# Kernel tuning notes

Measured on AMD Instinct MI355X. Metric: run time of the kernel, lower is better.

## Reference

```python
import jax, jax.numpy as jnp
import numpy as np
from jax import lax

B = 8          # batch
IMG = 224      # image size
PATCH = 16     # patch size / stride
D = 384        # embed_dim = d_model = d_inner (expand=1)
DEPTH = 24     # number of blocks
N = 16         # d_state
K = 4          # d_conv
R = 24         # dt_rank = ceil(D/16)
H = D * 4 * 2 // 3   # SwiGLU hidden = 1024
L = (IMG // PATCH) ** 2  # 196 tokens


def setup_inputs() -> dict:
    ks = iter(jax.random.split(jax.random.key(0), 40))
    def rn(shape, s=0.02):
        return jax.random.normal(next(ks), shape, jnp.float32) * s
    inp = {}
    inp["x"] = jax.random.normal(next(ks), (B, 3, IMG, IMG), jnp.float32)
    inp["patch_w"] = rn((D, 3, PATCH, PATCH))
    inp["patch_b"] = jnp.zeros((D,), jnp.float32)
    inp["norm1_w"] = jnp.ones((DEPTH, D), jnp.float32)
    inp["norm1_b"] = jnp.zeros((DEPTH, D), jnp.float32)
    inp["in_proj_w"] = rn((DEPTH, 2 * D, D))
    inp["conv_w"] = rn((DEPTH, D, K), 0.1)
    inp["conv_b"] = jnp.zeros((DEPTH, D), jnp.float32)
    inp["x_proj_w"] = rn((DEPTH, R + 2 * N, D))
    inp["dt_proj_w"] = rn((DEPTH, D, R), 0.1)
    inp["dt_proj_b"] = rn((DEPTH, D), 0.1)
    # S4D-real init: A = -exp(A_log), A_log = log(1..N)
    inp["A_log"] = jnp.tile(jnp.log(jnp.arange(1, N + 1, dtype=jnp.float32))[None, None, :], (DEPTH, D, 1))
    inp["D_skip"] = jnp.ones((DEPTH, D), jnp.float32)
    inp["out_proj_w"] = rn((DEPTH, D, D))
    inp["norm2_w"] = jnp.ones((DEPTH, D), jnp.float32)
    inp["norm2_b"] = jnp.zeros((DEPTH, D), jnp.float32)
    inp["w1_w"] = rn((DEPTH, H, D)); inp["w1_b"] = jnp.zeros((DEPTH, H), jnp.float32)
    inp["w2_w"] = rn((DEPTH, H, D)); inp["w2_b"] = jnp.zeros((DEPTH, H), jnp.float32)
    inp["w3_w"] = rn((DEPTH, D, H)); inp["w3_b"] = jnp.zeros((DEPTH, D), jnp.float32)
    inp["normf_w"] = jnp.ones((D,), jnp.float32)
    inp["normf_b"] = jnp.zeros((D,), jnp.float32)
    return inp


def _ln(x, w, b, eps=1e-5):
    m = x.mean(-1, keepdims=True)
    v = jnp.mean((x - m) ** 2, axis=-1, keepdims=True)
    return (x - m) / jnp.sqrt(v + eps) * w + b


def _mamba(x, in_w, cw, cb, xp_w, dtw, dtb, a_log, d_skip, ow):
    # x: [B, L, D]; Mamba with expand=1, bimamba 'none'
    bsz, seq, _ = x.shape
    xz = jnp.einsum('bld,ed->ble', x, in_w)        # [B, L, 2D]
    xc, z = jnp.split(xz, 2, axis=-1)
    # causal depthwise conv1d, kernel K, padding K-1, truncated to L
    xpd = jnp.pad(xc, ((0, 0), (K - 1, 0), (0, 0)))
    xconv = sum(xpd[:, k:k + seq, :] * cw[:, k] for k in range(K)) + cb
    xa = jax.nn.silu(xconv)
    dbc = jnp.einsum('bld,ed->ble', xa, xp_w)      # [B, L, R+2N]
    dt = jax.nn.softplus(jnp.einsum('blr,dr->bld', dbc[..., :R], dtw) + dtb)  # [B, L, D]
    Bm = dbc[..., R:R + N]                         # [B, L, N]
    Cm = dbc[..., R + N:]                          # [B, L, N]
    A = -jnp.exp(a_log)                            # [D, N]

    def step(h, t):
        dt_t, B_t, C_t, x_t = t                    # [B,D],[B,N],[B,N],[B,D]
        h = h * jnp.exp(dt_t[..., None] * A) + (dt_t * x_t)[..., None] * B_t[:, None, :]
        return h, jnp.einsum('bdn,bn->bd', h, C_t)

    h0 = jnp.zeros((bsz, D, N), x.dtype)
    _, ys = lax.scan(step, h0, (dt.transpose(1, 0, 2), Bm.transpose(1, 0, 2),
                                Cm.transpose(1, 0, 2), xa.transpose(1, 0, 2)))
    y = ys.transpose(1, 0, 2) + d_skip * xa
    y = y * jax.nn.silu(z)
    return jnp.einsum('bld,ed->ble', y, ow)


def _forward(x, patch_w, patch_b, norm1_w, norm1_b, in_proj_w, conv_w, conv_b,
             x_proj_w, dt_proj_w, dt_proj_b, A_log, D_skip, out_proj_w,
             norm2_w, norm2_b, w1_w, w1_b, w2_w, w2_b, w3_w, w3_b, normf_w, normf_b):
    p = lax.conv_general_dilated(x, patch_w, (PATCH, PATCH), 'VALID',
                                 dimension_numbers=('NCHW', 'OIHW', 'NCHW'))
    p = p + patch_b[None, :, None, None]
    h = p.reshape(p.shape[0], D, -1).transpose(0, 2, 1)   # [B, L, D]
    for i in range(DEPTH):
        h = h + _mamba(_ln(h, norm1_w[i], norm1_b[i]), in_proj_w[i], conv_w[i], conv_b[i],
                       x_proj_w[i], dt_proj_w[i], dt_proj_b[i], A_log[i], D_skip[i], out_proj_w[i])
        hn = _ln(h, norm2_w[i], norm2_b[i])
        hid = jax.nn.silu(hn @ w1_w[i].T + w1_b[i]) * (hn @ w2_w[i].T + w2_b[i])
        h = h + hid @ w3_w[i].T + w3_b[i]
    return _ln(h, normf_w, normf_b)


def reference(x, patch_w, patch_b, norm1_w, norm1_b, in_proj_w, conv_w, conv_b,
              x_proj_w, dt_proj_w, dt_proj_b, A_log, D_skip, out_proj_w,
              norm2_w, norm2_b, w1_w, w1_b, w2_w, w2_b, w3_w, w3_b, normf_w, normf_b):
    return _forward(x, patch_w, patch_b, norm1_w, norm1_b, in_proj_w, conv_w, conv_b,
                    x_proj_w, dt_proj_w, dt_proj_b, A_log, D_skip, out_proj_w,
                    norm2_w, norm2_b, w1_w, w1_b, w2_w, w2_b, w3_w, w3_b, normf_w, normf_b)
```

## Files before the change

kernel.cpp:

```cpp
#include <hip/hip_runtime.h>
#include <math.h>

#define BB 8
#define LL 196
#define DD 384
#define NDEPTH 24
#define NST 16
#define RRANK 24
#define HHID 1024
#define MROWS (BB*LL)
#define NCH 28
#define CHL 7

typedef float f32x4 __attribute__((ext_vector_type(4)));
typedef short s16x8 __attribute__((ext_vector_type(8)));
typedef short s16x4 __attribute__((ext_vector_type(4)));
typedef __bf16 b16x8 __attribute__((ext_vector_type(8)));
typedef unsigned short u16;
typedef unsigned int u32;

#if defined(__has_builtin)
#  if __has_builtin(__builtin_amdgcn_global_load_lds)
#    define HAS_GLL 1
#  endif
#endif
#ifndef HAS_GLL
#  define HAS_GLL 0
#endif

__device__ __forceinline__ float sigmoidf_(float x){ return 1.f/(1.f+__expf(-x)); }

__device__ __forceinline__ u16 f2bf(float f){
    u32 u = __builtin_bit_cast(u32, f);
    u32 r = (u + 0x7fffu + ((u >> 16) & 1u)) >> 16;
    return (u16)r;
}
__device__ __forceinline__ float bf2f(u16 v){
    u32 u = ((u32)v) << 16;
    return __builtin_bit_cast(float, u);
}

__device__ __forceinline__ void gll16(const u16* g, void* lds){
#if HAS_GLL
    __builtin_amdgcn_global_load_lds(
        (const __attribute__((address_space(1))) unsigned int*)g,
        (__attribute__((address_space(3))) unsigned int*)lds, 16, 0, 0);
#endif
}

template<typename V>
__device__ __forceinline__ auto mfma_try(V a, V b, f32x4 c, int)
    -> decltype(__builtin_amdgcn_mfma_f32_16x16x32_bf16(a, b, c, 0, 0, 0))
{ return __builtin_amdgcn_mfma_f32_16x16x32_bf16(a, b, c, 0, 0, 0); }

template<typename V>
__device__ __forceinline__ f32x4 mfma_try(V a, V b, f32x4 c, long)
{
    return __builtin_amdgcn_mfma_f32_16x16x32_bf16(
        __builtin_bit_cast(b16x8, a), __builtin_bit_cast(b16x8, b), c, 0, 0, 0);
}
__device__ __forceinline__ f32x4 mfma_bf16(s16x8 a, s16x8 b, f32x4 c){ return mfma_try(a, b, c, 0); }

__global__ __launch_bounds__(64) void ln_k(const float* __restrict__ X,
    const float* __restrict__ w, const float* __restrict__ b, float* __restrict__ Y)
{
    int row = blockIdx.x;
    int lane = threadIdx.x;
    const float* x = X + (size_t)row*DD;
    float v[6]; float s=0.f, s2=0.f;
    #pragma unroll
    for (int j=0;j<6;j++){ float t = x[lane + j*64]; v[j]=t; s+=t; s2+=t*t; }
    #pragma unroll
    for (int o=32;o>=1;o>>=1){ s += __shfl_xor(s,o); s2 += __shfl_xor(s2,o); }
    float m = s*(1.f/DD);
    float var = s2*(1.f/DD) - m*m;
    float rstd = rsqrtf(var + 1e-5f);
    #pragma unroll
    for (int j=0;j<6;j++){
        int c = lane + j*64;
        Y[(size_t)row*DD + c] = (v[j]-m)*rstd*w[c] + b[c];
    }
}

__global__ void gather_k(const float* __restrict__ x, u16* __restrict__ P)
{
    int idx = blockIdx.x*blockDim.x + threadIdx.x;
    if (idx >= MROWS*768) return;
    int k = idx % 768;
    int bl = idx / 768;
    int l = bl % LL;
    int b = bl / LL;
    int c = k >> 8;
    int rem = k & 255;
    int dy = rem >> 4, dx = rem & 15;
    int py = l / 14, px = l % 14;
    P[idx] = f2bf(x[(((size_t)b*3 + c)*224 + (py*16+dy))*224 + (px*16+dx)]);
}

__device__ __forceinline__ int swz(int row, int chunk){
    return (row << 7) + ((chunk ^ (row & 7)) << 4);
}

template<int EPI, bool WB, int CFG, int PRO, int K>
__global__ __launch_bounds__(256) void mgemm_k(
    const u16* __restrict__ A, const float* __restrict__ Af,
    const float* __restrict__ lnw, const float* __restrict__ lnb,
    const void* __restrict__ W1v, const void* __restrict__ W2v,
    const float* __restrict__ bias1, const float* __restrict__ bias2,
    float* __restrict__ Cf, u16* __restrict__ Cb,
    int M, int N)
{
    constexpr int  BM   = (CFG==1)?32:16;
    constexpr int  FM   = (CFG==2)?1:2;
    constexpr int  FN   = 2;
    constexpr int  NAR  = (BM+31)/32;
    constexpr bool DUAL = (EPI==4);
    constexpr int  ABY  = BM*128;
    constexpr int  BBY  = 128*128;
    constexpr bool ASY  = WB && (HAS_GLL==1);
    constexpr int  NKT  = K >> 6;
    __shared__ __attribute__((aligned(16))) char sm[2*ABY + 2*BBY + (DUAL ? 2*BBY : 0)];
    char* A0 = sm;          char* A1 = sm + ABY;
    char* B0 = sm + 2*ABY;  char* B1 = B0 + BBY;
    char* C0 = B1 + BBY;    char* C1 = C0 + BBY;

    const int tid = threadIdx.x;
    const int row0 = blockIdx.y * BM;
    const int col0 = blockIdx.x << 7;
    const int w = tid >> 6, lane = tid & 63;
    const int wn  = w;
    const int lr = lane & 15, lk = lane >> 4;
    const int ar0 = tid >> 3, ac8 = tid & 7;
    const bool apart = (CFG != 2) || (tid < 128);

    const u16*   W1b = (const u16*)W1v;
    const u16*   W2b = (const u16*)W2v;
    const float* W1f = (const float*)W1v;
    const float* W2f = (const float*)W2v;

    f32x4 acc [FM][FN] = {};
    f32x4 acc2[FM][FN] = {};

    s16x8 aval[NAR];
    s16x8 bval[4], b2val[4];
    float4 bvf[8], b2vf[8];
    s16x8 lnr[(PRO==1)?NKT:1];

    if (PRO == 1 && apart){
        const float* xrow = Af + (size_t)(row0 + ar0)*DD;
        float4 va[6], vb[6];
        float s = 0.f, s2 = 0.f;
        #pragma unroll
        for (int j=0;j<6;j++){
            va[j] = *(const float4*)(xrow + j*64 + ac8*8);
            vb[j] = *(const float4*)(xrow + j*64 + ac8*8 + 4);
            s  += va[j].x+va[j].y+va[j].z+va[j].w + vb[j].x+vb[j].y+vb[j].z+vb[j].w;
            s2 += va[j].x*va[j].x+va[j].y*va[j].y+va[j].z*va[j].z+va[j].w*va[j].w
                + vb[j].x*vb[j].x+vb[j].y*vb[j].y+vb[j].z*vb[j].z+vb[j].w*vb[j].w;
        }
        #pragma unroll
        for (int o=1;o<8;o<<=1){ s += __shfl_xor(s,o); s2 += __shfl_xor(s2,o); }
        float m = s*(1.f/DD);
        float rstd = rsqrtf(s2*(1.f/DD) - m*m + 1e-5f);
        #pragma unroll
        for (int j=0;j<6;j++){
            int c0 = j*64 + ac8*8;
            float4 w0 = *(const float4*)(lnw + c0);
            float4 w1 = *(const float4*)(lnw + c0 + 4);
            float4 b0 = *(const float4*)(lnb + c0);
            float4 b1 = *(const float4*)(lnb + c0 + 4);
            s16x8 ov;
            ov[0]=(short)f2bf((va[j].x-m)*rstd*w0.x+b0.x);
            ov[1]=(short)f2bf((va[j].y-m)*rstd*w0.y+b0.y);
            ov[2]=(short)f2bf((va[j].z-m)*rstd*w0.z+b0.z);
            ov[3]=(short)f2bf((va[j].w-m)*rstd*w0.w+b0.w);
            ov[4]=(short)f2bf((vb[j].x-m)*rstd*w1.x+b1.x);
            ov[5]=(short)f2bf((vb[j].y-m)*rstd*w1.y+b1.y);
            ov[6]=(short)f2bf((vb[j].z-m)*rstd*w1.z+b1.z);
            ov[7]=(short)f2bf((vb[j].w-m)*rstd*w1.w+b1.w);
            if (j < NKT) lnr[j] = ov;
        }
    }

    auto stageAsync = [&](int kt, char* bA, char* bB, char* bC){
        const int lhi = lane >> 3, llo = lane & 7;
        const int colel = (kt << 6) + ((llo ^ lhi) << 3);
        if (PRO == 0){
            constexpr int ACH = BM/8;
            #pragma unroll
            for (int ci = w; ci < ACH; ci += 4){
                int gr = row0 + ci*8 + lhi;
                gll16(A + (size_t)gr*K + colel, bA + ci*1024);
            }
        }
        #pragma unroll
        for (int i=0;i<4;i++){
            int ci = w*4 + i;
            int gb = col0 + ci*8 + lhi;
            gll16(W1b + (size_t)gb*K + colel, bB + ci*1024);
        }
        if (DUAL){
            #pragma unroll
            for (int i=0;i<4;i++){
                int ci = w*4 + i;
                int gb = col0 + ci*8 + lhi;
                gll16(W2b + (size_t)gb*K + colel, bC + ci*1024);
            }
        }
    };

    auto loadT = [&](int kt){
        const int kb = kt << 6;
        if (PRO == 0 && apart){
            #pragma unroll
            for (int i=0;i<NAR;i++){
                int gr = row0 + i*32 + ar0;
                if (gr < M) aval[i] = *(const s16x8*)(A + (size_t)gr*K + kb + ac8*8);
                else        aval[i] = s16x8{0,0,0,0,0,0,0,0};
            }
        }
        if (WB){
            #pragma unroll
            for (int i=0;i<4;i++){
                int gb = col0 + i*32 + ar0;
                if (gb < N) bval[i] = *(const s16x8*)(W1b + (size_t)gb*K + kb + ac8*8);
                else        bval[i] = s16x8{0,0,0,0,0,0,0,0};
            }
            if (DUAL){
                #pragma unroll
                for (int i=0;i<4;i++){
                    int gb = col0 + i*32 + ar0;
                    if (gb < N) b2val[i] = *(const s16x8*)(W2b + (size_t)gb*K + kb + ac8*8);
                    else        b2val[i] = s16x8{0,0,0,0,0,0,0,0};
                }
            }
        } else {
            #pragma unroll
            for (int i=0;i<8;i++){
                int ss = i*256 + tid;
                int r = ss >> 4, q = ss & 15;
                int gb = col0 + r;
                if (gb < N) bvf[i] = *(const float4*)(W1f + (size_t)gb*K + kb + q*4);
                else        bvf[i] = float4{0,0,0,0};
            }
            if (DUAL){
                #pragma unroll
                for (int i=0;i<8;i++){
                    int ss = i*256 + tid;
                    int r = ss >> 4, q = ss & 15;
                    int gb = col0 + r;
                    if (gb < N) b2vf[i] = *(const float4*)(W2f + (size_t)gb*K + kb + q*4);
                    else        b2vf[i] = float4{0,0,0,0};
                }
            }
        }
    };
    auto writeT = [&](char* bA, char* bB, char* bC){
        if (PRO == 0 && apart){
            #pragma unroll
            for (int i=0;i<NAR;i++)
                *(s16x8*)(bA + swz(i*32 + ar0, ac8)) = aval[i];
        }
        if (WB){
            #pragma unroll
            for (int i=0;i<4;i++)
                *(s16x8*)(bB + swz(i*32 + ar0, ac8)) = bval[i];
            if (DUAL){
                #pragma unroll
                for (int i=0;i<4;i++)
                    *(s16x8*)(bC + swz(i*32 + ar0, ac8)) = b2val[i];
            }
        } else {
            #pragma unroll
            for (int i=0;i<8;i++){
                int ss = i*256 + tid;
                int r = ss >> 4, q = ss & 15;
                float4 v = bvf[i];
                s16x4 cv = { (short)f2bf(v.x), (short)f2bf(v.y), (short)f2bf(v.z), (short)f2bf(v.w) };
                int off = (r << 7) + (((q >> 1) ^ (r & 7)) << 4) + ((q & 1) << 3);
                *(s16x4*)(bB + off) = cv;
            }
            if (DUAL){
                #pragma unroll
                for (int i=0;i<8;i++){
                    int ss = i*256 + tid;
                    int r = ss >> 4, q = ss & 15;
                    float4 v = b2vf[i];
                    s16x4 cv = { (short)f2bf(v.x), (short)f2bf(v.y), (short)f2bf(v.z), (short)f2bf(v.w) };
                    int off = (r << 7) + (((q >> 1) ^ (r & 7)) << 4) + ((q & 1) << 3);
                    *(s16x4*)(bC + off) = cv;
                }
            }
        }
    };

    auto compute = [&](char* cA, char* cB, char* cC){
        #pragma unroll
        for (int ks=0; ks<2; ks++){
            s16x8 af[FM], bfr[FN];
            #pragma unroll
            for (int m=0;m<FM;m++)
                af[m] = *(const s16x8*)(cA + swz(m*16 + lr, ks*4 + lk));
            #pragma unroll
            for (int n=0;n<FN;n++)
                bfr[n] = *(const s16x8*)(cB + swz(wn*32 + n*16 + lr, ks*4 + lk));
            #pragma unroll
            for (int m=0;m<FM;m++)
                #pragma unroll
                for (int n=0;n<FN;n++)
                    acc[m][n] = mfma_bf16(af[m], bfr[n], acc[m][n]);
            if (DUAL){
                s16x8 b2r[FN];
                #pragma unroll
                for (int n=0;n<FN;n++)
                    b2r[n] = *(const s16x8*)(cC + swz(wn*32 + n*16 + lr, ks*4 + lk));
                #pragma unroll
                for (int m=0;m<FM;m++)
                    #pragma unroll
                    for (int n=0;n<FN;n++)
                        acc2[m][n] = mfma_bf16(af[m], b2r[n], acc2[m][n]);
            }
        }
    };

    if (ASY) stageAsync(0, A0, B0, C0);
    else   { loadT(0); writeT(A0, B0, C0); }
    if (PRO == 1 && apart) *(s16x8*)(A0 + swz(ar0, ac8)) = lnr[0];
    __syncthreads();
    #pragma unroll
    for (int kt=0; kt<NKT; kt++){
        const bool more = (kt+1 < NKT);
        char* nA = (kt&1)?A0:A1; char* nB = (kt&1)?B0:B1; char* nC = (kt&1)?C0:C1;
        if (more){
            if (ASY) stageAsync(kt+1, nA, nB, nC);
            else     loadT(kt+1);
            if (PRO == 1 && apart) *(s16x8*)(nA + swz(ar0, ac8)) = lnr[(kt+1 < NKT) ? (kt+1) : 0];
        }
        if (kt & 1) compute(A1, B1, C1);
        else        compute(A0, B0, C0);
        if (more && !ASY) writeT(nA, nB, nC);
        __syncthreads();
    }

    #pragma unroll
    for (int n=0;n<FN;n++){
        int gc = col0 + wn*32 + n*16 + lr;
        if (gc >= N) continue;
        float b1 = 0.f, b2 = 0.f;
        if (EPI==1||EPI==3||EPI==4) b1 = bias1[gc];
        if (EPI==4) b2 = bias2[gc];
        #pragma unroll
        for (int m=0;m<FM;m++){
            #pragma unroll
            for (int r=0;r<4;r++){
                int gr = row0 + m*16 + lk*4 + r;
                if (gr >= M) continue;
                float v = acc[m][n][r];
                if (EPI==1||EPI==3) v += b1;
                if (EPI==2||EPI==3) v += Cf[(size_t)gr*N + gc];
                if (EPI==4){
                    float v1 = v + b1;
                    float v2 = acc2[m][n][r] + b2;
                    Cb[(size_t)gr*N + gc] = f2bf(v1 * sigmoidf_(v1) * v2);
                } else if (EPI==6){
                    Cb[(size_t)gr*N + gc] = f2bf(v);
                } else {
                    Cf[(size_t)gr*N + gc] = v;
                }
            }
        }
    }
}

template<int K>
__device__ __forceinline__ int off_a(int row, int chunk){
    return row*(K*2) + ((chunk ^ (row & 7)) << 4);
}

template<bool WB>
__global__ __launch_bounds__(256) void xproj_k(
    const u16* __restrict__ xzb,
    const float* __restrict__ cw, const float* __restrict__ cb,
    const void* __restrict__ Wv,
    float* __restrict__ dbc)
{
    constexpr int K = DD, N = 56;
    constexpr int ABY = 16*K*2;
    __shared__ __attribute__((aligned(16))) char sm[ABY + 2*16384];
    char* sA = sm;
    char* B0 = sm + ABY;
    char* B1 = B0 + 16384;

    const int tid = threadIdx.x;
    const int row0 = blockIdx.x * 16;
    const int wv = tid >> 6, lane = tid & 63;
    const int lr = lane & 15, lk = lane >> 4;
    const int ar0 = tid >> 3, ac8 = tid & 7;

    const u16*   Wb = (const u16*)Wv;
    const float* Wf = (const float*)Wv;

    f32x4 acc[2] = {};
    s16x8 bval[4];
    float4 bvf[8];

    auto loadB = [&](int kt){
        const int kb = kt << 6;
        if (WB){
            #pragma unroll
            for (int i=0;i<4;i++){
                int gb = i*32 + ar0;
                if (gb < N) bval[i] = *(const s16x8*)(Wb + (size_t)gb*K + kb + ac8*8);
                else        bval[i] = s16x8{0,0,0,0,0,0,0,0};
            }
        } else {
            #pragma unroll
            for (int i=0;i<8;i++){
                int ss = i*256 + tid;
                int r = ss >> 4, q = ss & 15;
                if (r < N) bvf[i] = *(const float4*)(Wf + (size_t)r*K + kb + q*4);
                else       bvf[i] = float4{0,0,0,0};
            }
        }
    };
    auto writeB = [&](char* bB){
        if (WB){
            #pragma unroll
            for (int i=0;i<4;i++)
                *(s16x8*)(bB + swz(i*32 + ar0, ac8)) = bval[i];
        } else {
            #pragma unroll
            for (int i=0;i<8;i++){
                int ss = i*256 + tid;
                int r = ss >> 4, q = ss & 15;
                float4 v = bvf[i];
                s16x4 cv = { (short)f2bf(v.x), (short)f2bf(v.y), (short)f2bf(v.z), (short)f2bf(v.w) };
                int off = (r << 7) + (((q >> 1) ^ (r & 7)) << 4) + ((q & 1) << 3);
                *(s16x4*)(bB + off) = cv;
            }
        }
    };

    loadB(0);

    #pragma unroll
    for (int r=0;r<4;r++){
        int rl = wv*4 + r, gr = row0 + rl;
        if (lane < 48){
            int l = gr % LL, bb = gr / LL;
            int d0 = lane*8;
            float a[8];
            #pragma unroll
            for (int j=0;j<8;j++) a[j] = cb[d0+j];
            #pragma unroll
            for (int t=0;t<4;t++){
                int ls = l - 3 + t;
                if (ls >= 0){
                    s16x8 xv = *(const s16x8*)(xzb + (size_t)(bb*LL+ls)*768 + d0);
                    #pragma unroll
                    for (int j=0;j<8;j++)
                        a[j] = fmaf(bf2f((u16)xv[j]), cw[(d0+j)*4+t], a[j]);
                }
            }
            s16x8 ov;
            #pragma unroll
            for (int j=0;j<8;j++)
                ov[j] = (short)f2bf(a[j]*sigmoidf_(a[j]));
            *(s16x8*)(sA + off_a<K>(rl, lane)) = ov;
        }
    }

    writeB(B0);
    __syncthreads();

    constexpr int nkt = K >> 6;
    #pragma unroll
    for (int kt=0; kt<nkt; kt++){
        const bool more = (kt+1 < nkt);
        if (more) loadB(kt+1);
        char* cB = (kt & 1) ? B1 : B0;
        #pragma unroll
        for (int ks=0; ks<2; ks++){
            s16x8 af = *(const s16x8*)(sA + off_a<K>(lr, kt*8 + ks*4 + lk));
            #pragma unroll
            for (int n=0;n<2;n++){
                s16x8 bfr = *(const s16x8*)(cB + swz(wv*32 + n*16 + lr, ks*4 + lk));
                acc[n] = mfma_bf16(af, bfr, acc[n]);
            }
        }
        if (more) writeB((kt & 1) ? B0 : B1);
        __syncthreads();
    }

    #pragma unroll
    for (int n=0;n<2;n++){
        int gc = wv*32 + n*16 + lr;
        if (gc >= N) continue;
        #pragma unroll
        for (int r=0;r<4;r++){
            int gr = row0 + lk*4 + r;
            dbc[(size_t)gr*N + gc] = acc[n][r];
        }
    }
}

__global__ void cvtw_k(const float* __restrict__ s, u16* __restrict__ d, int n)
{
    int i = blockIdx.x*blockDim.x + threadIdx.x;
    int idx = i*4;
    if (idx + 4 <= n){
        float4 v = *(const float4*)(s + idx);
        s16x4 cv = { (short)f2bf(v.x), (short)f2bf(v.y), (short)f2bf(v.z), (short)f2bf(v.w) };
        *(s16x4*)(d + idx) = cv;
    } else {
        for (int j=idx;j<n;j++) d[j] = f2bf(s[j]);
    }
}

__global__ __launch_bounds__(384) void scanA_k(
    const float* __restrict__ dbc, const u16* __restrict__ xzb,
    const float* __restrict__ cw, const float* __restrict__ cb,
    const float* __restrict__ dtw, const float* __restrict__ dtb,
    const float* __restrict__ a_log,
    float* __restrict__ Pout, float* __restrict__ Sout,
    float2* __restrict__ dtxv)
{
    int b = blockIdx.x / NCH;
    int c = blockIdx.x % NCH;
    int d = threadIdx.x;
    __shared__ float Ds[CHL][56];
    for (int t = threadIdx.x; t < CHL*56; t += 384){
        int j = t/56, q = t%56;
        Ds[j][q] = dbc[(size_t)(b*LL + c*CHL + j)*56 + q];
    }
    __syncthreads();
    float cwr[4];
    #pragma unroll
    for (int k=0;k<4;k++) cwr[k] = cw[d*4+k];
    float cbv = cb[d];
    float dtwr[RRANK];
    #pragma unroll
    for (int r=0;r<RRANK;r++) dtwr[r] = dtw[d*RRANK + r];
    float dtbv = dtb[d];
    float Aa[NST];
    #pragma unroll
    for (int n=0;n<NST;n++) Aa[n] = -__expf(a_log[d*NST+n]);
    int l0 = c*CHL;
    float p3=0.f, p2=0.f, p1=0.f;
    if (l0 >= 3) p3 = bf2f(xzb[(size_t)(b*LL+l0-3)*768 + d]);
    if (l0 >= 2) p2 = bf2f(xzb[(size_t)(b*LL+l0-2)*768 + d]);
    if (l0 >= 1) p1 = bf2f(xzb[(size_t)(b*LL+l0-1)*768 + d]);
    float hst[NST], P[NST];
    #pragma unroll
    for (int n=0;n<NST;n++){ hst[n]=0.f; P[n]=1.f; }
    #pragma unroll
    for (int j=0;j<CHL;j++){
        int row = b*LL + l0 + j;
        float cur = bf2f(xzb[(size_t)row*768 + d]);
        float a = cbv;
        a = fmaf(p3, cwr[0], a); a = fmaf(p2, cwr[1], a);
        a = fmaf(p1, cwr[2], a); a = fmaf(cur, cwr[3], a);
        p3 = p2; p2 = p1; p1 = cur;
        float xv = a * sigmoidf_(a);
        float t = dtbv;
        #pragma unroll
        for (int r=0;r<RRANK;r++) t = fmaf(dtwr[r], Ds[j][r], t);
        float dtv = (t > 20.f) ? t : log1pf(__expf(t));
        dtxv[(size_t)row*DD + d] = float2{dtv, xv};
        float du = dtv*xv;
        #pragma unroll
        for (int n=0;n<NST;n++){
            float e = __expf(dtv*Aa[n]);
            hst[n] = fmaf(hst[n], e, du*Ds[j][24+n]);
            P[n] *= e;
        }
    }
    size_t base = ((size_t)(b*NCH + c)*DD + d)*NST;
    #pragma unroll
    for (int n=0;n<NST;n++){ Pout[base+n]=P[n]; Sout[base+n]=hst[n]; }
}

__global__ __launch_bounds__(384) void scanC_k(
    const float* __restrict__ dbc, const float2* __restrict__ dtxv,
    const u16* __restrict__ xzb, const float* __restrict__ a_log,
    const float* __restrict__ Pin, const float* __restrict__ Sin,
    const float* __restrict__ dskip,
    u16* __restrict__ yg)
{
    int b = blockIdx.x / NCH;
    int c = blockIdx.x % NCH;
    int d = threadIdx.x;
    __shared__ float Ds[CHL][56];
    for (int t = threadIdx.x; t < CHL*56; t += 384){
        int j = t/56, q = t%56;
        Ds[j][q] = dbc[(size_t)(b*LL + c*CHL + j)*56 + q];
    }
    __syncthreads();
    float hst[NST];
    #pragma unroll
    for (int n=0;n<NST;n++) hst[n]=0.f;
    for (int cc=0; cc<c; cc++){
        size_t base = ((size_t)(b*NCH + cc)*DD + d)*NST;
        #pragma unroll
        for (int n=0;n<NST;n++)
            hst[n] = fmaf(Pin[base+n], hst[n], Sin[base+n]);
    }
    float Aa[NST];
    #pragma unroll
    for (int n=0;n<NST;n++) Aa[n] = -__expf(a_log[d*NST+n]);
    float dsk = dskip[d];
    int l0 = c*CHL;
    #pragma unroll
    for (int j=0;j<CHL;j++){
        int row = b*LL + l0 + j;
        float2 dx = dtxv[(size_t)row*DD + d];
        float dtv = dx.x, xv = dx.y;
        float du = dtv*xv;
        float y = 0.f;
        #pragma unroll
        for (int n=0;n<NST;n++){
            float e = __expf(dtv*Aa[n]);
            hst[n] = fmaf(hst[n], e, du*Ds[j][24+n]);
            y = fmaf(hst[n], Ds[j][40+n], y);
        }
        float zv = bf2f(xzb[(size_t)row*768 + 384 + d]);
        float g = zv * sigmoidf_(zv);
        yg[(size_t)row*DD + d] = f2bf((y + dsk*xv)*g);
    }
}

template<int EPI, int CFG, int PRO, int K>
static void mg(bool wb, dim3 g, hipStream_t s,
               const void* A, const float* Af, const float* lnw, const float* lnb,
               const void* Wb, const void* Wf, const void* W2b, const void* W2f,
               const float* b1, const float* b2, float* Cf, u16* Cb,
               int M, int N)
{
    if (wb) mgemm_k<EPI,true ,CFG,PRO,K><<<g,256,0,s>>>((const u16*)A, Af, lnw, lnb, Wb, W2b, b1, b2, Cf, Cb, M, N);
    else    mgemm_k<EPI,false,CFG,PRO,K><<<g,256,0,s>>>((const u16*)A, Af, lnw, lnb, Wf, W2f, b1, b2, Cf, Cb, M, N);
}

extern "C" void kernel_launch(void* const* d_in, const int* in_sizes, int n_in,
                              void* d_out, int out_size, void* d_ws, size_t ws_size,
                              hipStream_t stream)
{
    const float* x         = (const float*)d_in[0];
    const float* patch_w   = (const float*)d_in[1];
    const float* patch_b   = (const float*)d_in[2];
    const float* norm1_w   = (const float*)d_in[3];
    const float* norm1_b   = (const float*)d_in[4];
    const float* in_proj_w = (const float*)d_in[5];
    const float* conv_w    = (const float*)d_in[6];
    const float* conv_b    = (const float*)d_in[7];
    const float* x_proj_w  = (const float*)d_in[8];
    const float* dt_w      = (const float*)d_in[9];
    const float* dt_b      = (const float*)d_in[10];
    const float* A_log     = (const float*)d_in[11];
    const float* D_skip    = (const float*)d_in[12];
    const float* out_w     = (const float*)d_in[13];
    const float* norm2_w   = (const float*)d_in[14];
    const float* norm2_b   = (const float*)d_in[15];
    const float* w1_w      = (const float*)d_in[16];
    const float* w1_b      = (const float*)d_in[17];
    const float* w2_w      = (const float*)d_in[18];
    const float* w2_b      = (const float*)d_in[19];
    const float* w3_w      = (const float*)d_in[20];
    const float* w3_b      = (const float*)d_in[21];
    const float* normf_w   = (const float*)d_in[22];
    const float* normf_b   = (const float*)d_in[23];

    char* wsb = (char*)d_ws;
    size_t o = 0;
    auto take = [&](size_t bytes) -> char* {
        char* p = wsb + o;
        o += (bytes + 255) & ~(size_t)255;
        return p;
    };

    float* h    = (float*)take((size_t)602112*4);
    float* dbc  = (float*)take((size_t)87808*4);
    float* Pb   = (float*)take((size_t)BB*NCH*DD*NST*4);
    float* Sb   = (float*)take((size_t)BB*NCH*DD*NST*4);
    float2* dtxv= (float2*)take((size_t)MROWS*DD*8);
    u16*  xzb   = (u16*)take((size_t)1204224*2);
    u16*  yg    = (u16*)take((size_t)602112*2);
    u16*  hid   = (u16*)take((size_t)1605632*2);
    u16*  patches = hid;

    const size_t NPW = 294912, NIN = 7077888, NOUT = 3538944,
                 NW1 = 9437184, NW2 = 9437184, NW3 = 9437184, NXP = 516096;
    u16* wcP = (u16*)take(NPW*2);
    u16* wcI = (u16*)take(NIN*2);
    u16* wcO = (u16*)take(NOUT*2);
    u16* wc1 = (u16*)take(NW1*2);
    u16* wc2 = (u16*)take(NW2*2);
    u16* wc3 = (u16*)take(NW3*2);
    u16* wcX = (u16*)take(NXP*2);
    bool wb = (ws_size >= o);

    if (wb){
        cvtw_k<<<(int)((NPW/4+255)/256), 256, 0, stream>>>(patch_w, wcP, (int)NPW);
        cvtw_k<<<(int)((NIN/4+255)/256), 256, 0, stream>>>(in_proj_w, wcI, (int)NIN);
        cvtw_k<<<(int)((NOUT/4+255)/256),256, 0, stream>>>(out_w, wcO, (int)NOUT);
        cvtw_k<<<(int)((NW1/4+255)/256), 256, 0, stream>>>(w1_w, wc1, (int)NW1);
        cvtw_k<<<(int)((NW2/4+255)/256), 256, 0, stream>>>(w2_w, wc2, (int)NW2);
        cvtw_k<<<(int)((NW3/4+255)/256), 256, 0, stream>>>(w3_w, wc3, (int)NW3);
        cvtw_k<<<(int)((NXP/4+255)/256), 256, 0, stream>>>(x_proj_w, wcX, (int)NXP);
    }

    const int GY32 = MROWS/32;
    const int GY16 = MROWS/16;

    gather_k<<<(MROWS*768+255)/256, 256, 0, stream>>>(x, patches);
    mg<1,2,0,768>(wb, dim3(3,GY16), stream, patches, nullptr, nullptr, nullptr,
              wcP, patch_w, nullptr, nullptr, patch_b, nullptr, h, nullptr, MROWS, DD);

    for (int i=0;i<NDEPTH;i++){
        mg<6,1,1,384>(wb, dim3(6,GY32), stream, nullptr, h, norm1_w + i*DD, norm1_b + i*DD,
                  wcI + (size_t)i*768*DD, in_proj_w + (size_t)i*768*DD, nullptr, nullptr,
                  nullptr, nullptr, nullptr, xzb, MROWS, 768);
        if (wb) xproj_k<true ><<<GY16, 256, 0, stream>>>(xzb, conv_w + i*DD*4, conv_b + i*DD,
                                                         wcX + (size_t)i*56*DD, dbc);
        else    xproj_k<false><<<GY16, 256, 0, stream>>>(xzb, conv_w + i*DD*4, conv_b + i*DD,
                                                         x_proj_w + (size_t)i*56*DD, dbc);
        scanA_k<<<BB*NCH, 384, 0, stream>>>(dbc, xzb, conv_w + i*DD*4, conv_b + i*DD,
                                            dt_w + (size_t)i*DD*RRANK, dt_b + i*DD,
                                            A_log + (size_t)i*DD*NST, Pb, Sb, dtxv);
        scanC_k<<<BB*NCH, 384, 0, stream>>>(dbc, dtxv, xzb, A_log + (size_t)i*DD*NST,
                                            Pb, Sb, D_skip + i*DD, yg);
        mg<2,2,0,384>(wb, dim3(3,GY16), stream, yg, nullptr, nullptr, nullptr,
                  wcO + (size_t)i*DD*DD, out_w + (size_t)i*DD*DD, nullptr, nullptr,
                  nullptr, nullptr, h, nullptr, MROWS, DD);
        mg<4,1,1,384>(wb, dim3(8,GY32), stream, nullptr, h, norm2_w + i*DD, norm2_b + i*DD,
                  wc1 + (size_t)i*HHID*DD, w1_w + (size_t)i*HHID*DD,
                  wc2 + (size_t)i*HHID*DD, w2_w + (size_t)i*HHID*DD,
                  w1_b + i*HHID, w2_b + i*HHID, nullptr, hid, MROWS, HHID);
        mg<3,2,0,1024>(wb, dim3(3,GY16), stream, hid, nullptr, nullptr, nullptr,
                  wc3 + (size_t)i*DD*HHID, w3_w + (size_t)i*DD*HHID, nullptr, nullptr,
                  w3_b + i*DD, nullptr, h, nullptr, MROWS, DD);
    }

    ln_k<<<MROWS, 64, 0, stream>>>(h, normf_w, normf_b, (float*)d_out);
}
```

Baseline: 2.434 ms.

## Prefetch two K-tiles ahead with partial vmcnt waits in async GEMM path

The async (global_load_lds) GEMM path now issues loads for the first two K tiles before computing. Each iteration then releases the buffer with a barrier, issues the load for tile kt+2 into it, and waits with a partial vmcnt count so the next tile's loads can still be in flight. This is meant to hide global-to-LDS latency better than the previous single-ahead prefetch followed by a full __syncthreads. It relies on hand-written s_waitcnt counts (4 or 8) matching the number of outstanding loads per stage, which is fragile if the load count differs.

```diff
diff --git a/kernel.cpp b/kernel.cpp
--- a/kernel.cpp
+++ b/kernel.cpp
@@ -46,6 +46,18 @@
         (const __attribute__((address_space(1))) unsigned int*)g,
         (__attribute__((address_space(3))) unsigned int*)lds, 16, 0, 0);
 #endif
+}
+
+template<int N> __device__ __forceinline__ void waitbar(){
+    if constexpr (N==0) asm volatile("s_waitcnt vmcnt(0) lgkmcnt(0)\ns_barrier" ::: "memory");
+    else if constexpr (N==4) asm volatile("s_waitcnt vmcnt(4) lgkmcnt(0)\ns_barrier" ::: "memory");
+    else if constexpr (N==8) asm volatile("s_waitcnt vmcnt(8) lgkmcnt(0)\ns_barrier" ::: "memory");
+    else asm volatile("s_waitcnt vmcnt(0) lgkmcnt(0)\ns_barrier" ::: "memory");
+    __builtin_amdgcn_sched_barrier(0);
+}
+__device__ __forceinline__ void bar_release(){
+    asm volatile("s_waitcnt lgkmcnt(0)\ns_barrier" ::: "memory");
+    __builtin_amdgcn_sched_barrier(0);
 }
 
 template<typename V>
@@ -119,6 +131,7 @@
     constexpr int  BBY  = 128*128;
     constexpr bool ASY  = WB && (HAS_GLL==1);
     constexpr int  NKT  = K >> 6;
+    constexpr int  NLW  = DUAL ? 8 : 4;
     __shared__ __attribute__((aligned(16))) char sm[2*ABY + 2*BBY + (DUAL ? 2*BBY : 0)];
     char* A0 = sm;          char* A1 = sm + ABY;
     char* B0 = sm + 2*ABY;  char* B1 = B0 + BBY;
@@ -323,23 +336,48 @@
         }
     };
 
-    if (ASY) stageAsync(0, A0, B0, C0);
-    else   { loadT(0); writeT(A0, B0, C0); }
-    if (PRO == 1 && apart) *(s16x8*)(A0 + swz(ar0, ac8)) = lnr[0];
-    __syncthreads();
-    #pragma unroll
-    for (int kt=0; kt<NKT; kt++){
-        const bool more = (kt+1 < NKT);
-        char* nA = (kt&1)?A0:A1; char* nB = (kt&1)?B0:B1; char* nC = (kt&1)?C0:C1;
-        if (more){
-            if (ASY) stageAsync(kt+1, nA, nB, nC);
-            else     loadT(kt+1);
-            if (PRO == 1 && apart) *(s16x8*)(nA + swz(ar0, ac8)) = lnr[(kt+1 < NKT) ? (kt+1) : 0];
-        }
-        if (kt & 1) compute(A1, B1, C1);
-        else        compute(A0, B0, C0);
-        if (more && !ASY) writeT(nA, nB, nC);
+    if (ASY){
+        stageAsync(0, A0, B0, C0);
+        if (NKT > 1) stageAsync(1, A1, B1, C1);
+        if (PRO == 1 && apart){
+            *(s16x8*)(A0 + swz(ar0, ac8)) = lnr[0];
+            if (NKT > 1) *(s16x8*)(A1 + swz(ar0, ac8)) = lnr[(1 < NKT) ? 1 : 0];
+        }
+        if (NKT > 1) waitbar<NLW>(); else waitbar<0>();
+        #pragma unroll
+        for (int kt=0; kt<NKT; kt++){
+            if (kt & 1) compute(A1, B1, C1);
+            else        compute(A0, B0, C0);
+            if (kt+1 < NKT){
+                bar_release();
+                if (kt+2 < NKT){
+                    char* rA = (kt&1)?A1:A0; char* rB = (kt&1)?B1:B0; char* rC = (kt&1)?C1:C0;
+                    stageAsync(kt+2, rA, rB, rC);
+                    if (PRO == 1 && apart)
+                        *(s16x8*)(rA + swz(ar0, ac8)) = lnr[(kt+2 < NKT) ? (kt+2) : 0];
+                    waitbar<NLW>();
+                } else {
+                    waitbar<0>();
+                }
+            }
+        }
+    } else {
+        loadT(0); writeT(A0, B0, C0);
+        if (PRO == 1 && apart) *(s16x8*)(A0 + swz(ar0, ac8)) = lnr[0];
         __syncthreads();
+        #pragma unroll
+        for (int kt=0; kt<NKT; kt++){
+            const bool more = (kt+1 < NKT);
+            char* nA = (kt&1)?A0:A1; char* nB = (kt&1)?B0:B1; char* nC = (kt&1)?C0:C1;
+            if (more){
+                loadT(kt+1);
+                if (PRO == 1 && apart) *(s16x8*)(nA + swz(ar0, ac8)) = lnr[(kt+1 < NKT) ? (kt+1) : 0];
+            }
+            if (kt & 1) compute(A1, B1, C1);
+            else        compute(A0, B0, C0);
+            if (more) writeT(nA, nB, nC);
+            __syncthreads();
+        }
     }
 
     #pragma unroll
```

New measurement: 2.408 ms. Within noise of the previous version (-1.1%).
